# Optimization experiments

Measured on AMD Instinct MI355X. Metric: run time of the kernel, lower is better.

The kernel has to match this reference:

```python
import jax, jax.numpy as jnp
import numpy as np

_W = jnp.array([10., 9., 8., 7., 6., 5., 4., 3., 2., 1.], dtype=jnp.float32)
_W_NORM = _W / jnp.sum(_W)  # np.average normalizes by weight sum (55)


def setup_inputs() -> dict:
    key = jax.random.key(0)
    k1, k2 = jax.random.split(key)
    x = jax.random.randint(k1, (1024, 64, 10), 0, 8000, dtype=jnp.int32)
    table = jax.random.normal(k2, (8000, 256), dtype=jnp.float32)
    return {"x": x, "table": table}


def reference(x, table):
    # Gather per-char vectors: [T, F, 10, D]
    vecs = table[x]
    # Weighted average over the 10 chars (weights [10..1], normalized)
    return jnp.einsum('tfcd,c->tfd', vecs, _W_NORM)
```

## Files before the change

kernel.cpp:

```cpp
#include <hip/hip_runtime.h>
#include <hip/hip_fp16.h>


#define ROWS_TOTAL (1024 * 64)
#define TROWS 8000
#define TD 256

typedef float v4f __attribute__((ext_vector_type(4)));
typedef _Float16 h8 __attribute__((ext_vector_type(8)));

__global__ __launch_bounds__(256)
void cvt_perm(const float* __restrict__ t, _Float16* __restrict__ o) {
    const int tid = blockIdx.x * 256 + threadIdx.x;
    const int row = tid >> 5;
    const int m   = tid & 31;
    const float* src = t + (size_t)row * TD + 4 * m;
    v4f a = *reinterpret_cast<const v4f*>(src);
    v4f b = *reinterpret_cast<const v4f*>(src + 128);
    h8 r;
    r[0] = (_Float16)a.x; r[1] = (_Float16)a.y;
    r[2] = (_Float16)a.z; r[3] = (_Float16)a.w;
    r[4] = (_Float16)b.x; r[5] = (_Float16)b.y;
    r[6] = (_Float16)b.z; r[7] = (_Float16)b.w;
    __builtin_nontemporal_store(r, reinterpret_cast<h8*>(o + (size_t)tid * 8));
}

__global__ __launch_bounds__(256)
void char2vec_hw(const int* __restrict__ x,
                 const _Float16* __restrict__ tb,
                 float* __restrict__ out) {
    const int l    = threadIdx.x & 63;
    const int wave = threadIdx.x >> 6;
    const int row0 = (blockIdx.x * 4 + wave) * 2;
    const int half = l >> 5;
    const int m    = l & 31;
    const int row  = row0 + half;

    const int t = x[row0 * 10 + (l < 20 ? l : 19)];

    int idx[10];
#pragma unroll
    for (int c = 0; c < 10; ++c) idx[c] = __shfl(t, half * 10 + c);

    h8 v[10];
#pragma unroll
    for (int c = 0; c < 10; ++c)
        v[c] = *reinterpret_cast<const h8*>(tb + (size_t)idx[c] * TD + m * 8);

    const float w[10] = {10.f / 55.f, 9.f / 55.f, 8.f / 55.f, 7.f / 55.f,
                         6.f / 55.f,  5.f / 55.f, 4.f / 55.f, 3.f / 55.f,
                         2.f / 55.f,  1.f / 55.f};

    float acc[8] = {0, 0, 0, 0, 0, 0, 0, 0};
#pragma unroll
    for (int c = 0; c < 10; ++c) {
#pragma unroll
        for (int e = 0; e < 8; ++e)
            acc[e] = fmaf((float)v[c][e], w[c], acc[e]);
    }

    v4f lo = {acc[0], acc[1], acc[2], acc[3]};
    v4f hi = {acc[4], acc[5], acc[6], acc[7]};
    float* orow = out + (size_t)row * TD;
    __builtin_nontemporal_store(lo, reinterpret_cast<v4f*>(orow + 4 * m));
    __builtin_nontemporal_store(hi, reinterpret_cast<v4f*>(orow + 128 + 4 * m));
}

__global__ __launch_bounds__(256)
void char2vec_sliced2(const int* __restrict__ x,
                      const float* __restrict__ table,
                      float* __restrict__ out) {
    const int slice = blockIdx.x & 7;
    const int rgrp  = blockIdx.x >> 3;
    const int wave  = threadIdx.x >> 6;
    const int lane  = threadIdx.x & 63;

    const int row0 = rgrp * 64 + wave * 16 + (lane >> 3) * 2;
    const int row1 = row0 + 1;
    const int d    = slice * 32 + (lane & 7) * 4;

    const int2* __restrict__ xa = reinterpret_cast<const int2*>(x + row0 * 10);
    const int2* __restrict__ xb = reinterpret_cast<const int2*>(x + row1 * 10);
    int2 pa[5], pb[5];
#pragma unroll
    for (int i = 0; i < 5; ++i) pa[i] = xa[i];
#pragma unroll
    for (int i = 0; i < 5; ++i) pb[i] = xb[i];

    int ia[10], ib[10];
#pragma unroll
    for (int i = 0; i < 5; ++i) {
        ia[2 * i] = pa[i].x; ia[2 * i + 1] = pa[i].y;
        ib[2 * i] = pb[i].x; ib[2 * i + 1] = pb[i].y;
    }

    v4f va[10], vb[10];
#pragma unroll
    for (int c = 0; c < 10; ++c)
        va[c] = *reinterpret_cast<const v4f*>(table + (size_t)ia[c] * TD + d);
#pragma unroll
    for (int c = 0; c < 10; ++c)
        vb[c] = *reinterpret_cast<const v4f*>(table + (size_t)ib[c] * TD + d);

    const float w[10] = {10.f / 55.f, 9.f / 55.f, 8.f / 55.f, 7.f / 55.f,
                         6.f / 55.f,  5.f / 55.f, 4.f / 55.f, 3.f / 55.f,
                         2.f / 55.f,  1.f / 55.f};

    v4f acc0 = (v4f)0.0f, acc1 = (v4f)0.0f;
#pragma unroll
    for (int c = 0; c < 10; ++c) {
        acc0 += va[c] * w[c];
        acc1 += vb[c] * w[c];
    }

    __builtin_nontemporal_store(
        acc0, reinterpret_cast<v4f*>(out + (size_t)row0 * TD + d));
    __builtin_nontemporal_store(
        acc1, reinterpret_cast<v4f*>(out + (size_t)row1 * TD + d));
}

extern "C" void kernel_launch(void* const* d_in, const int* in_sizes, int n_in,
                              void* d_out, int out_size, void* d_ws, size_t ws_size,
                              hipStream_t stream) {
    const int*   x     = (const int*)d_in[0];
    const float* table = (const float*)d_in[1];
    float*       out   = (float*)d_out;

    const size_t f16_bytes = (size_t)TROWS * TD * sizeof(_Float16);

    if (ws_size >= f16_bytes) {
        _Float16* tb = (_Float16*)d_ws;
        cvt_perm<<<(TROWS * 32) / 256, 256, 0, stream>>>(table, tb);
        char2vec_hw<<<ROWS_TOTAL / 8, 256, 0, stream>>>(x, tb, out);
    } else {
        const int blocks = (ROWS_TOTAL / 64) * 8;
        char2vec_sliced2<<<blocks, 256, 0, stream>>>(x, table, out);
    }
}
```

Measured before the change: 31.60 us.

## Split fp16 table rows into halves so each wave gathers half-rows for four rows

The fp16 table permutation is changed so that each 128-column half of a row is stored contiguously. The main kernel now has each wave cover four output rows over one column half, using 16 lanes per row, and alternating blocks take the two halves. Each gather therefore reads a 256-byte half-row segment, and each wave loads four rows' index sets with one load. The output stores switch from nontemporal to regular stores, which may change how writes interact with the cache.

```diff
diff --git a/kernel.cpp b/kernel.cpp
--- a/kernel.cpp
+++ b/kernel.cpp
@@ -10,13 +10,14 @@
 typedef _Float16 h8 __attribute__((ext_vector_type(8)));
 
 __global__ __launch_bounds__(256)
-void cvt_perm(const float* __restrict__ t, _Float16* __restrict__ o) {
+void cvt_perm2(const float* __restrict__ t, _Float16* __restrict__ o) {
     const int tid = blockIdx.x * 256 + threadIdx.x;
     const int row = tid >> 5;
-    const int m   = tid & 31;
-    const float* src = t + (size_t)row * TD + 4 * m;
+    const int s   = (tid >> 4) & 1;
+    const int i   = tid & 15;
+    const float* src = t + (size_t)row * TD + s * 128 + 4 * i;
     v4f a = *reinterpret_cast<const v4f*>(src);
-    v4f b = *reinterpret_cast<const v4f*>(src + 128);
+    v4f b = *reinterpret_cast<const v4f*>(src + 64);
     h8 r;
     r[0] = (_Float16)a.x; r[1] = (_Float16)a.y;
     r[2] = (_Float16)a.z; r[3] = (_Float16)a.w;
@@ -26,26 +27,29 @@
 }
 
 __global__ __launch_bounds__(256)
-void char2vec_hw(const int* __restrict__ x,
+void char2vec_w2(const int* __restrict__ x,
                  const _Float16* __restrict__ tb,
                  float* __restrict__ out) {
-    const int l    = threadIdx.x & 63;
-    const int wave = threadIdx.x >> 6;
-    const int row0 = (blockIdx.x * 4 + wave) * 2;
-    const int half = l >> 5;
-    const int m    = l & 31;
-    const int row  = row0 + half;
+    const int l  = threadIdx.x & 63;
+    const int wv = threadIdx.x >> 6;
+    const int q  = l >> 4;
+    const int i  = l & 15;
 
-    const int t = x[row0 * 10 + (l < 20 ? l : 19)];
+    const int s       = blockIdx.x & 1;
+    const int rowbase = (blockIdx.x >> 1) * 16 + wv * 4;
+    const int row     = rowbase + q;
+
+    const int t = x[rowbase * 10 + (l < 40 ? l : 39)];
 
     int idx[10];
 #pragma unroll
-    for (int c = 0; c < 10; ++c) idx[c] = __shfl(t, half * 10 + c);
+    for (int c = 0; c < 10; ++c) idx[c] = __shfl(t, q * 10 + c);
 
     h8 v[10];
 #pragma unroll
     for (int c = 0; c < 10; ++c)
-        v[c] = *reinterpret_cast<const h8*>(tb + (size_t)idx[c] * TD + m * 8);
+        v[c] = *reinterpret_cast<const h8*>(
+            tb + (size_t)idx[c] * TD + s * 128 + i * 8);
 
     const float w[10] = {10.f / 55.f, 9.f / 55.f, 8.f / 55.f, 7.f / 55.f,
                          6.f / 55.f,  5.f / 55.f, 4.f / 55.f, 3.f / 55.f,
@@ -61,9 +65,9 @@
 
     v4f lo = {acc[0], acc[1], acc[2], acc[3]};
     v4f hi = {acc[4], acc[5], acc[6], acc[7]};
-    float* orow = out + (size_t)row * TD;
-    __builtin_nontemporal_store(lo, reinterpret_cast<v4f*>(orow + 4 * m));
-    __builtin_nontemporal_store(hi, reinterpret_cast<v4f*>(orow + 128 + 4 * m));
+    float* orow = out + (size_t)row * TD + s * 128;
+    *reinterpret_cast<v4f*>(orow + 4 * i)      = lo;
+    *reinterpret_cast<v4f*>(orow + 64 + 4 * i) = hi;
 }
 
 __global__ __launch_bounds__(256)
@@ -130,8 +134,8 @@
 
     if (ws_size >= f16_bytes) {
         _Float16* tb = (_Float16*)d_ws;
-        cvt_perm<<<(TROWS * 32) / 256, 256, 0, stream>>>(table, tb);
-        char2vec_hw<<<ROWS_TOTAL / 8, 256, 0, stream>>>(x, tb, out);
+        cvt_perm2<<<(TROWS * 32) / 256, 256, 0, stream>>>(table, tb);
+        char2vec_w2<<<(ROWS_TOTAL / 16) * 2, 256, 0, stream>>>(x, tb, out);
     } else {
         const int blocks = (ROWS_TOTAL / 64) * 8;
         char2vec_sliced2<<<blocks, 256, 0, stream>>>(x, table, out);
```

Result: faster. 29.59 us (-6.4%).
